# Optimization experiments

Hardware: AMD Instinct MI355X
Metric: run time of the kernel (lower is better)

The kernel has to match this reference:

```python
import math
import jax, jax.numpy as jnp
import numpy as np

DIM = 4096
N_HEADS = 32
N_KV_HEADS = 8
HEAD_DIM = DIM // N_HEADS        # 128
N_REP = N_HEADS // N_KV_HEADS    # 4
BSZ = 1
SEQ = 2048
ROPE_THETA = 500000.0


def setup_inputs() -> dict:
    key = jax.random.key(0)
    ks = jax.random.split(key, 5)
    scale = 1.0 / math.sqrt(DIM)
    x = jax.random.normal(ks[0], (BSZ, SEQ, DIM), dtype=jnp.float32)
    wq = jax.random.normal(ks[1], (N_HEADS * HEAD_DIM, DIM), dtype=jnp.float32) * scale
    wk = jax.random.normal(ks[2], (N_KV_HEADS * HEAD_DIM, DIM), dtype=jnp.float32) * scale
    wv = jax.random.normal(ks[3], (N_KV_HEADS * HEAD_DIM, DIM), dtype=jnp.float32) * scale
    wo = jax.random.normal(ks[4], (N_HEADS * HEAD_DIM, DIM), dtype=jnp.float32).T * scale
    wo = jnp.asarray(wo)  # [DIM, N_HEADS*HEAD_DIM] like nn.Linear(in=heads*hd, out=dim).weight
    # RoPE tables: freqs_cis[t, j] = exp(i * t * theta^{-2j/head_dim}), j in [0, head_dim/2)
    inv_freq = 1.0 / (ROPE_THETA ** (np.arange(0, HEAD_DIM, 2, dtype=np.float32) / HEAD_DIM))
    t = np.arange(SEQ, dtype=np.float32)
    ang = np.outer(t, inv_freq)  # [SEQ, HEAD_DIM//2]
    freqs_cos = jnp.asarray(np.cos(ang), dtype=jnp.float32)
    freqs_sin = jnp.asarray(np.sin(ang), dtype=jnp.float32)
    # additive causal mask [SEQ, SEQ]
    mask = jnp.where(jnp.tril(jnp.ones((SEQ, SEQ), dtype=bool)), 0.0, -1e9).astype(jnp.float32)
    return {"x": x, "wq": wq, "wk": wk, "wv": wv, "wo": wo,
            "freqs_cos": freqs_cos, "freqs_sin": freqs_sin, "mask": mask}


def _apply_rope(xh, cos, sin):
    # xh: [b, s, h, head_dim]; cos/sin: [s, head_dim//2]
    b, s, h, d = xh.shape
    xr = xh.reshape(b, s, h, d // 2, 2)
    x0, x1 = xr[..., 0], xr[..., 1]
    c = cos[None, :, None, :]
    sn = sin[None, :, None, :]
    o0 = x0 * c - x1 * sn
    o1 = x0 * sn + x1 * c
    return jnp.stack([o0, o1], axis=-1).reshape(b, s, h, d)


def reference(x, wq, wk, wv, wo, freqs_cos, freqs_sin, mask):
    bsz, seqlen, _ = x.shape
    xq = (x @ wq.T).reshape(bsz, seqlen, N_HEADS, HEAD_DIM)
    xk = (x @ wk.T).reshape(bsz, seqlen, N_KV_HEADS, HEAD_DIM)
    xv = (x @ wv.T).reshape(bsz, seqlen, N_KV_HEADS, HEAD_DIM)
    xq = _apply_rope(xq, freqs_cos, freqs_sin)
    xk = _apply_rope(xk, freqs_cos, freqs_sin)
    # repeat_kv (GQA expansion)
    keys = jnp.repeat(xk, N_REP, axis=2)    # [b, s, N_HEADS, hd]
    values = jnp.repeat(xv, N_REP, axis=2)
    scores = jnp.einsum('bqhd,bkhd->bhqk', xq, keys) / math.sqrt(HEAD_DIM)
    scores = scores + mask[None, None, :, :]
    scores = jax.nn.softmax(scores.astype(jnp.float32), axis=-1).astype(xq.dtype)
    out = jnp.einsum('bhqk,bkhd->bqhd', scores, values)
    out = out.reshape(bsz, seqlen, N_HEADS * HEAD_DIM)
    return out @ wo.T
```

## Files before the change

kernel.cpp:

```cpp
#include <hip/hip_runtime.h>
#include <math.h>
#include <stdint.h>
#include <stddef.h>


typedef __attribute__((ext_vector_type(8))) short bf16x8;
typedef __attribute__((ext_vector_type(4))) short bf16x4;
typedef __attribute__((ext_vector_type(4))) float f32x4;
typedef unsigned short u16;
typedef unsigned int u32;

#define NEG_BIG (-1.0e9f)
#define MFMA32(a, b, c) __builtin_amdgcn_mfma_f32_16x16x32_bf16(a, b, c, 0, 0, 0)
#define SFENCE() __builtin_amdgcn_sched_barrier(0)
#define BAR() __builtin_amdgcn_s_barrier()
#define VMW(n_) asm volatile("s_waitcnt vmcnt(" #n_ ")" ::: "memory")

__device__ __forceinline__ float bf2f(u16 b) {
    return __uint_as_float(((unsigned int)b) << 16);
}
__device__ __forceinline__ u16 f2bf(float f) {
    unsigned int u = __float_as_uint(f);
    u += 0x7fff + ((u >> 16) & 1);
    return (u16)(u >> 16);
}
__device__ __forceinline__ void gld_lds16(short* lds, const u16* g) {
    __builtin_amdgcn_global_load_lds(
        (const __attribute__((address_space(1))) void*)g,
        (__attribute__((address_space(3))) void*)lds, 16, 0, 0);
}
__device__ __forceinline__ void cvt8(const float* __restrict__ s,
                                     u16* __restrict__ d, int i) {
    float4 a, c;
    __builtin_memcpy(&a, s + i, 16);
    __builtin_memcpy(&c, s + i + 4, 16);
    bf16x8 o;
    o[0] = (short)f2bf(a.x); o[1] = (short)f2bf(a.y);
    o[2] = (short)f2bf(a.z); o[3] = (short)f2bf(a.w);
    o[4] = (short)f2bf(c.x); o[5] = (short)f2bf(c.y);
    o[6] = (short)f2bf(c.z); o[7] = (short)f2bf(c.w);
    __builtin_memcpy(d + i, &o, 16);
}

__global__ __launch_bounds__(256) void cvt_all(
    const float* __restrict__ x, const float* __restrict__ wq,
    const float* __restrict__ wk, const float* __restrict__ wv,
    u16* __restrict__ xb, u16* __restrict__ wqb, u16* __restrict__ wkb,
    u16* __restrict__ wvb) {
    const int b = blockIdx.x;
    const float* s; u16* d; int off;
    if (b < 4096)       { s = x;  d = xb;  off = b; }
    else if (b < 12288) { s = wq; d = wqb; off = b - 4096; }
    else if (b < 14336) { s = wk; d = wkb; off = b - 12288; }
    else                { s = wv; d = wvb; off = b - 14336; }
    cvt8(s, d, off * 2048 + threadIdx.x * 8);
}


#define QSTGA(bf_, ks_, kt_)                                                 \
    { _Pragma("unroll") for (int r_ = 0; r_ < 2; ++r_)                       \
        gld_lds16(Ad + (bf_) * 16384 + (ks_) * 8192 + r_ * 4096,             \
                  Ag + gK * r_ + (size_t)(kt_) * 64 + (ks_) * 32); }
#define QSTGB(bf_, ks_, kt_)                                                 \
    { _Pragma("unroll") for (int r_ = 0; r_ < 2; ++r_)                       \
        gld_lds16(Bd + (bf_) * 16384 + (ks_) * 8192 + r_ * 4096,             \
                  Bg + gK * r_ + (size_t)(kt_) * 64 + (ks_) * 32); }
#define QRDA(bank_, bf_, ks_, mh_)                                           \
    { _Pragma("unroll") for (int i_ = 0; i_ < 4; ++i_)                       \
        __builtin_memcpy(&bank_[i_], S + (bf_) * 16384 + (ks_) * 8192 +      \
                         abase + ((mh_) * 64 + i_ * 16) * 32, 16); }
#define QRDB(bank_, bf_, ks_)                                                \
    { _Pragma("unroll") for (int n_ = 0; n_ < 4; ++n_)                       \
        __builtin_memcpy(&bank_[n_], Bs + (bf_) * 16384 + (ks_) * 8192 +     \
                         bbase + n_ * 512, 16); }
#define QMM(afb_, bfb_, mh_)                                                 \
    {                                                                        \
        __builtin_amdgcn_s_setprio(1);                                       \
        _Pragma("unroll") for (int i_ = 0; i_ < 4; ++i_)                     \
            _Pragma("unroll") for (int n_ = 0; n_ < 4; ++n_)                 \
                acc[(mh_) * 4 + i_][n_] =                                    \
                    MFMA32(afb_[i_], bfb_[n_], acc[(mh_) * 4 + i_][n_]);     \
        __builtin_amdgcn_s_setprio(0);                                       \
    }

template <int OUT, int ROPE>
__device__ __forceinline__ void gemm_q(const u16* __restrict__ A,
                                       const u16* __restrict__ B,
                                       void* __restrict__ C,
                                       const float* __restrict__ fc,
                                       const float* __restrict__ fs,
                                       int mb, int nb, int N, int K,
                                       short* __restrict__ S) {
    short* const Bs = S + 32768;
    const int t = threadIdx.x;
    const int lane = t & 63, l15 = lane & 15, quad = lane >> 4;
    const int wid = t >> 6, wr = wid >> 2, wc = wid & 3;

    const int srow = t >> 2;
    const int cs = (t & 3) ^ ((t >> 3) & 3);
    const u16* const Ag = A + (size_t)(mb * 256 + srow) * K + cs * 8;
    const u16* const Bg = B + (size_t)(nb * 256 + srow) * K + cs * 8;
    short* const Ad = S + t * 8;
    short* const Bd = Bs + t * 8;
    const size_t gK = (size_t)128 * K;

    const int swz = (quad ^ ((l15 >> 1) & 3)) * 8;
    const int abase = (wr * 128 + l15) * 32 + swz;
    const int bbase = (wc * 64 + l15) * 32 + swz;

    f32x4 acc[8][4] = {};
    bf16x8 af0[4], af1[4], bf0[4], bf1[4];

    QSTGA(0, 0, 0); QSTGB(0, 0, 0);
    QSTGA(0, 1, 0); QSTGB(0, 1, 0);
    QSTGA(1, 0, 1); QSTGB(1, 0, 1);
    VMW(8);
    BAR();
    QRDA(af0, 0, 0, 0); QRDB(bf0, 0, 0);
    SFENCE();

    const int nIt = K >> 7;
    for (int it = 0; it < nIt - 1; ++it) {
        const int k1 = 2 * it + 1, kn0 = 2 * it + 2, kn1 = 2 * it + 3;
        QSTGA(1, 1, k1);  QRDA(af1, 0, 0, 1);                    QMM(af0, bf0, 0); SFENCE(); VMW(6); BAR();
        QSTGB(1, 1, k1);  QRDA(af0, 0, 1, 0); QRDB(bf1, 0, 1);   QMM(af1, bf0, 1); SFENCE();         BAR();
        QSTGA(0, 0, kn0); QRDA(af1, 0, 1, 1);                    QMM(af0, bf1, 0); SFENCE(); VMW(6); BAR();
        QSTGB(0, 0, kn0); QRDA(af0, 1, 0, 0); QRDB(bf0, 1, 0);   QMM(af1, bf1, 1); SFENCE();         BAR();
        QSTGA(0, 1, kn0); QRDA(af1, 1, 0, 1);                    QMM(af0, bf0, 0); SFENCE(); VMW(6); BAR();
        QSTGB(0, 1, kn0); QRDA(af0, 1, 1, 0); QRDB(bf1, 1, 1);   QMM(af1, bf0, 1); SFENCE();         BAR();
        QSTGA(1, 0, kn1); QRDA(af1, 1, 1, 1);                    QMM(af0, bf1, 0); SFENCE(); VMW(6); BAR();
        QSTGB(1, 0, kn1); QRDA(af0, 0, 0, 0); QRDB(bf0, 0, 0);   QMM(af1, bf1, 1); SFENCE();         BAR();
    }
    {
        const int k1 = 2 * nIt - 1;
        QSTGA(1, 1, k1);  QRDA(af1, 0, 0, 1);                    QMM(af0, bf0, 0); SFENCE(); VMW(6); BAR();
        QSTGB(1, 1, k1);  QRDA(af0, 0, 1, 0); QRDB(bf1, 0, 1);   QMM(af1, bf0, 1); SFENCE();         BAR();
        QRDA(af1, 0, 1, 1);                                      QMM(af0, bf1, 0); SFENCE(); VMW(4); BAR();
        QRDA(af0, 1, 0, 0); QRDB(bf0, 1, 0);                     QMM(af1, bf1, 1); SFENCE();         BAR();
        QRDA(af1, 1, 0, 1);                                      QMM(af0, bf0, 0); SFENCE(); VMW(0); BAR();
        QRDA(af0, 1, 1, 0); QRDB(bf1, 1, 1);                     QMM(af1, bf0, 1); SFENCE();         BAR();
        QRDA(af1, 1, 1, 1);                                      QMM(af0, bf1, 0); SFENCE();         BAR();
        QMM(af1, bf1, 1);
    }

#pragma unroll
    for (int i8 = 0; i8 < 8; ++i8) {
        const int rowb = mb * 256 + wr * 128 + (i8 >> 2) * 64 +
                         (i8 & 3) * 16 + quad * 4;
#pragma unroll
        for (int j = 0; j < 4; ++j) {
            const int col = nb * 256 + wc * 64 + j * 16 + l15;
            if (OUT == 2) {
                bf16x4 v;
#pragma unroll
                for (int r = 0; r < 4; ++r) v[r] = (short)f2bf(acc[i8][j][r]);
                __builtin_memcpy((u16*)C + (size_t)col * 2048 + rowb, &v, 8);
            } else if (ROPE) {
                const int pi = (col & 127) >> 1;
                const bool odd = (l15 & 1);
#pragma unroll
                for (int r = 0; r < 4; ++r) {
                    const int s = rowb + r;
                    const float c = fc[s * 64 + pi];
                    const float sn = fs[s * 64 + pi];
                    const float v = acc[i8][j][r];
                    const float vp = __shfl_xor(v, 1);
                    const float out = odd ? (vp * sn + v * c)
                                          : (v * c - vp * sn);
                    ((u16*)C)[(size_t)s * N + col] = f2bf(out);
                }
            } else {
#pragma unroll
                for (int r = 0; r < 4; ++r)
                    ((u16*)C)[(size_t)(rowb + r) * N + col] =
                        f2bf(acc[i8][j][r]);
            }
        }
    }
}

__global__ __launch_bounds__(512, 2) void qkv_proj8(
    const u16* __restrict__ x,
    const u16* __restrict__ wq, const u16* __restrict__ wk,
    const u16* __restrict__ wv,
    const float* __restrict__ wof, u16* __restrict__ wob,
    const float* __restrict__ fc, const float* __restrict__ fs,
    u16* __restrict__ Q, u16* __restrict__ Kc, u16* __restrict__ Vt) {
    __shared__ __align__(16) short S[65536];
    const int lid = blockIdx.x;
    if (lid >= 192) {
        const int cb = lid - 192, t = threadIdx.x;
        for (int it = 0; it < 64; ++it)
            cvt8(wof, wob, ((cb * 64 + it) * 512 + t) * 8);
        return;
    }
    const int swzb = (lid & 7) * 24 + (lid >> 3);
    const int mb = swzb & 7, y = swzb >> 3;
    if (y < 16)
        gemm_q<0, 1>(x, wq, Q, fc, fs, mb, y, 4096, 4096, S);
    else if (y < 20)
        gemm_q<0, 1>(x, wk, Kc, fc, fs, mb, y - 16, 1024, 4096, S);
    else
        gemm_q<2, 0>(x, wv, Vt, fc, fs, mb, y - 20, 1024, 4096, S);
}


#define O8_STG(bf_, ks_, kt_)                                                \
    {                                                                        \
        gld_lds16(Ad + (bf_) * 8192 + (ks_) * 4096,                          \
                  Ag + (size_t)(kt_) * 64 + (ks_) * 32);                     \
        _Pragma("unroll") for (int r_ = 0; r_ < 2; ++r_)                     \
            gld_lds16(Bd + (bf_) * 16384 + (ks_) * 8192 + r_ * 4096,         \
                      Bg + gK * r_ + (size_t)(kt_) * 64 + (ks_) * 32);       \
    }
#define O8_PHASE(bf_, ks_, STAGE_, WAIT_)                                    \
    {                                                                        \
        _Pragma("unroll") for (int n_ = 0; n_ < 4; ++n_)                     \
            __builtin_memcpy(&bfr[n_], Bs + (bf_) * 16384 + (ks_) * 8192 +   \
                                           bbase + n_ * 512, 16);            \
        _Pragma("unroll") for (int i_ = 0; i_ < 4; ++i_)                     \
            __builtin_memcpy(&af[i_], S + (bf_) * 8192 + (ks_) * 4096 +      \
                                          abase + i_ * 512, 16);             \
        STAGE_;                                                              \
        SFENCE();                                                            \
        __builtin_amdgcn_s_barrier();                                        \
        asm volatile("s_waitcnt lgkmcnt(0)" ::: "memory");                   \
        SFENCE();                                                            \
        __builtin_amdgcn_s_setprio(1);                                       \
        _Pragma("unroll") for (int i_ = 0; i_ < 4; ++i_)                     \
            _Pragma("unroll") for (int n_ = 0; n_ < 4; ++n_)                 \
                acc[i_][n_] = MFMA32(af[i_], bfr[n_], acc[i_][n_]);          \
        __builtin_amdgcn_s_setprio(0);                                       \
        SFENCE();                                                            \
        WAIT_;                                                               \
        __builtin_amdgcn_s_barrier();                                        \
    }

__global__ __launch_bounds__(512, 2) void oproj8(
    const u16* __restrict__ A, const u16* __restrict__ wo,
    float* __restrict__ out) {
    __shared__ __align__(16) short S[49152];
    short* const Bs = S + 16384;
    const int lid = blockIdx.x;
    const int logical = (lid & 7) * 32 + (lid >> 3);
    const int mb = logical & 15, nb = logical >> 4;

    const int t = threadIdx.x;
    const int lane = t & 63, l15 = lane & 15, quad = lane >> 4;
    const int wid = t >> 6, wr = wid >> 2, wc = wid & 3;

    const int srow = t >> 2;
    const int cs = (t & 3) ^ ((t >> 3) & 3);
    const u16* const Ag = A + (size_t)(mb * 128 + srow) * 4096 + cs * 8;
    const u16* const Bg = wo + (size_t)(nb * 256 + srow) * 4096 + cs * 8;
    short* const Ad = S + t * 8;
    short* const Bd = Bs + t * 8;
    const size_t gK = (size_t)128 * 4096;

    const int swz = (quad ^ ((l15 >> 1) & 3)) * 8;
    const int abase = (wr * 64 + l15) * 32 + swz;
    const int bbase = (wc * 64 + l15) * 32 + swz;

    f32x4 acc[4][4] = {};
    bf16x8 af[4], bfr[4];

    O8_STG(0, 0, 0); O8_STG(0, 1, 0); O8_STG(1, 0, 1);
    VMW(6);
    BAR();

    const int nIt = 32;
    for (int it = 0; it < nIt - 1; ++it) {
        const int k1 = 2 * it + 1, kn0 = 2 * it + 2, kn1 = 2 * it + 3;
        O8_PHASE(0, 0, O8_STG(1, 1, k1),  VMW(6));
        O8_PHASE(0, 1, O8_STG(0, 0, kn0), VMW(6));
        O8_PHASE(1, 0, O8_STG(0, 1, kn0), VMW(6));
        O8_PHASE(1, 1, O8_STG(1, 0, kn1), VMW(6));
    }
    {
        const int k1 = 2 * nIt - 1;
        O8_PHASE(0, 0, O8_STG(1, 1, k1), VMW(6));
        O8_PHASE(0, 1, ,                 VMW(3));
        O8_PHASE(1, 0, ,                 VMW(0));
        O8_PHASE(1, 1, , );
    }

#pragma unroll
    for (int i = 0; i < 4; ++i) {
        const int rowb = mb * 128 + wr * 64 + i * 16 + quad * 4;
#pragma unroll
        for (int j = 0; j < 4; ++j) {
            const int col = nb * 256 + wc * 64 + j * 16 + l15;
#pragma unroll
            for (int r = 0; r < 4; ++r)
                out[(size_t)(rowb + r) * 4096 + col] = acc[i][j][r];
        }
    }
}

__device__ __forceinline__ int kswz(int row, int cs) {
    int f = (row & 3) | ((row & 8) >> 1);
    return row * 128 + ((cs ^ f) << 3);
}

template <bool MASKED>
__device__ __forceinline__ void fa_step_lds(
    const short* __restrict__ Kl, const short* __restrict__ Vl,
    int kb, int kadd, int q0, int l15, int quad,
    const int (&koff)[8], const int (&voff)[8],
    const bf16x8 (&qf)[4], const bf16x8 vones,
    f32x4 (&o)[8], f32x4& o9, float& m) {
    const float c1 = 0.08838834764831845f * 1.4426950408889634f;

    bf16x8 kf[8];
#pragma unroll
    for (int i = 0; i < 8; ++i)
        __builtin_memcpy(&kf[i], Kl + koff[i] + kadd, 16);
    f32x4 s0 = {0, 0, 0, 0}, s1 = {0, 0, 0, 0};
#pragma unroll
    for (int c = 0; c < 4; ++c) {
        s0 = MFMA32(kf[c], qf[c], s0);
        s1 = MFMA32(kf[4 + c], qf[c], s1);
    }

    bf16x8 vf[8];
#pragma unroll
    for (int n = 0; n < 8; ++n) __builtin_memcpy(&vf[n], Vl + voff[n], 16);

    float sv0[4], sv1[4];
    const int q = q0 + l15;
#pragma unroll
    for (int r = 0; r < 4; ++r) {
        sv0[r] = s0[r];
        sv1[r] = s1[r];
        if (MASKED) {
            if (kb + 8 * quad + r > q) sv0[r] = NEG_BIG;
            if (kb + 8 * quad + 4 + r > q) sv1[r] = NEG_BIG;
        }
    }

    float mx = fmaxf(fmaxf(fmaxf(sv0[0], sv0[1]), fmaxf(sv0[2], sv0[3])),
                     fmaxf(fmaxf(sv1[0], sv1[1]), fmaxf(sv1[2], sv1[3])));
    mx = fmaxf(mx, __shfl_xor(mx, 16));
    mx = fmaxf(mx, __shfl_xor(mx, 32));

    if (!__all(mx <= m + 90.0f)) {
        float mnew = fmaxf(m, mx);
        float alpha = exp2f((m - mnew) * c1);
        float aO[4];
#pragma unroll
        for (int r = 0; r < 4; ++r) aO[r] = __shfl(alpha, quad * 20 + r);
#pragma unroll
        for (int n = 0; n < 8; ++n)
#pragma unroll
            for (int r = 0; r < 4; ++r) o[n][r] *= aO[r];
#pragma unroll
        for (int r = 0; r < 4; ++r) o9[r] *= aO[r];
        m = mnew;
    }

    const float mc = m * c1;
    float p0[4], p1[4];
#pragma unroll
    for (int r = 0; r < 4; ++r) {
        p0[r] = exp2f(__builtin_fmaf(sv0[r], c1, -mc));
        p1[r] = exp2f(__builtin_fmaf(sv1[r], c1, -mc));
    }

    u32 w0, w1, w2, w3;
    asm("v_cvt_pk_bf16_f32 %0, %1, %2" : "=v"(w0) : "v"(p0[0]), "v"(p0[1]));
    asm("v_cvt_pk_bf16_f32 %0, %1, %2" : "=v"(w1) : "v"(p0[2]), "v"(p0[3]));
    asm("v_cvt_pk_bf16_f32 %0, %1, %2" : "=v"(w2) : "v"(p1[0]), "v"(p1[1]));
    asm("v_cvt_pk_bf16_f32 %0, %1, %2" : "=v"(w3) : "v"(p1[2]), "v"(p1[3]));
    u32 wa[4] = {w0, w1, w2, w3};
    bf16x8 pa;
    __builtin_memcpy(&pa, wa, 16);

#pragma unroll
    for (int n = 0; n < 8; ++n) o[n] = MFMA32(pa, vf[n], o[n]);
    o9 = MFMA32(pa, vones, o9);
}

__device__ __forceinline__ void fa_task(
    const u16* __restrict__ Q, const u16* __restrict__ Kc,
    const u16* __restrict__ Vt, u16* __restrict__ O,
    short* __restrict__ Kl0, short* __restrict__ Vl0,
    int q0, int nbt64, int h, int kvh, int t) {
    const int lane = t & 63;
    const int l15 = lane & 15, quad = lane >> 4;

    bf16x8 qf[4];
    const u16* qp = Q + (size_t)(q0 + l15) * 4096 + h * 128 + quad * 8;
#pragma unroll
    for (int c = 0; c < 4; ++c) __builtin_memcpy(&qf[c], qp + c * 32, 16);

    bf16x8 vones;
#pragma unroll
    for (int i = 0; i < 8; ++i) vones[i] = (short)0x3F80;

    const u16* ksrc[4]; short* kdst[4];
    const u16* vsrc[4]; short* vdst[4];
#pragma unroll
    for (int r = 0; r < 4; ++r) {
        int row = (t >> 4) + 16 * r;
        int slot = t & 15;
        int f = (row & 3) | ((row & 8) >> 1);
        int cks = slot ^ f;
        ksrc[r] = Kc + (size_t)row * 1024 + kvh * 128 + cks * 8;
        kdst[r] = Kl0 + (t + 256 * r) * 8;
        int rowv = (t >> 3) + 32 * r;
        int csv = (t & 7) ^ ((t >> 3) & 7);
        vsrc[r] = Vt + (size_t)(kvh * 128 + rowv) * 2048 + csv * 8;
        vdst[r] = Vl0 + (t + 256 * r) * 8;
    }

    const int rk0 = 8 * (l15 >> 2) + (l15 & 3);
    int koff[8], voff0[8], voff1[8];
#pragma unroll
    for (int c = 0; c < 4; ++c) {
        koff[c] = kswz(rk0, quad + c * 4);
        koff[4 + c] = kswz(rk0 + 4, quad + c * 4);
    }
#pragma unroll
    for (int n = 0; n < 8; ++n) {
        const int row = n * 16 + l15;
        voff0[n] = row * 64 + ((quad ^ (l15 & 7)) << 3);
        voff1[n] = row * 64 + (((quad + 4) ^ (l15 & 7)) << 3);
    }

    f32x4 o[8] = {};
    f32x4 o9 = {0, 0, 0, 0};
    float m = NEG_BIG;
    const int my_nb32 = (q0 + 47) / 32;

#pragma unroll
    for (int r = 0; r < 4; ++r) {
        gld_lds16(kdst[r], ksrc[r]);
        gld_lds16(vdst[r], vsrc[r]);
    }
    __syncthreads();

    for (int ib = 0; ib < nbt64; ++ib) {
        if (ib + 1 < nbt64) {
            const int kb = (ib + 1) * 64;
            const int bo = ((ib + 1) & 1) * 8192;
#pragma unroll
            for (int r = 0; r < 4; ++r) {
                gld_lds16(kdst[r] + bo, ksrc[r] + (size_t)kb * 1024);
                gld_lds16(vdst[r] + bo, vsrc[r] + kb);
            }
        }
        const short* Kl = Kl0 + (ib & 1) * 8192;
        const short* Vl = Vl0 + (ib & 1) * 8192;
#pragma unroll
        for (int sub = 0; sub < 2; ++sub) {
            const int ib32 = 2 * ib + sub;
            if (ib32 < my_nb32) {
                const int kb = ib * 64 + sub * 32;
                const int kadd = sub * 4096;
                if (ib32 == my_nb32 - 1)
                    fa_step_lds<true>(Kl, Vl, kb, kadd, q0, l15, quad, koff,
                                      sub ? voff1 : voff0, qf, vones, o, o9,
                                      m);
                else
                    fa_step_lds<false>(Kl, Vl, kb, kadd, q0, l15, quad, koff,
                                       sub ? voff1 : voff0, qf, vones, o, o9,
                                       m);
            }
        }
        __syncthreads();
    }

    float inv[4];
#pragma unroll
    for (int r = 0; r < 4; ++r) inv[r] = 1.f / o9[r];
#pragma unroll
    for (int n = 0; n < 8; ++n)
#pragma unroll
        for (int r = 0; r < 4; ++r) {
            int row = q0 + quad * 4 + r;
            O[(size_t)row * 4096 + h * 128 + n * 16 + l15] =
                f2bf(o[n][r] * inv[r]);
        }
}

__global__ __launch_bounds__(256, 2) void flash_attn(
    const u16* __restrict__ Q, const u16* __restrict__ Kc,
    const u16* __restrict__ Vt, u16* __restrict__ O) {
    __shared__ __align__(16) short Kl[2 * 64 * 128];
    __shared__ __align__(16) short Vl[2 * 128 * 64];
    const int id = blockIdx.x;
    const int c = id & 7;
    const int j = id >> 3;
    const int h = 4 * c + (j & 3);
    const int pp = j >> 2;
    const int kvh = c;
    const int t = threadIdx.x, wave = t >> 6;
    fa_task(Q, Kc, Vt, O, Kl, Vl, pp * 64 + wave * 16, pp + 1, h, kvh, t);
    const int tb = 31 - pp;
    fa_task(Q, Kc, Vt, O, Kl, Vl, tb * 64 + (3 - wave) * 16, tb + 1, h,
            kvh, t);
}

extern "C" void kernel_launch(void* const* d_in, const int* in_sizes, int n_in,
                              void* d_out, int out_size, void* d_ws,
                              size_t ws_size, hipStream_t stream) {
    const float* x  = (const float*)d_in[0];
    const float* wq = (const float*)d_in[1];
    const float* wk = (const float*)d_in[2];
    const float* wv = (const float*)d_in[3];
    const float* wo = (const float*)d_in[4];
    const float* fc = (const float*)d_in[5];
    const float* fs = (const float*)d_in[6];
    float* out = (float*)d_out;

    const int NX = 2048 * 4096;
    const int NQW = 4096 * 4096;
    const int NKW = 1024 * 4096;
    const int NKV = 2048 * 1024;

    u16* Q   = (u16*)d_ws;
    u16* Kc  = Q   + NX;
    u16* Vt  = Kc  + NKV;
    u16* Ao  = Vt  + NKV;
    u16* xb  = Ao  + NX;
    u16* wqb = xb  + NX;
    u16* wkb = wqb + NQW;
    u16* wvb = wkb + NKW;
    u16* wob = wvb + NKW;

    cvt_all<<<16384, 256, 0, stream>>>(x, wq, wk, wv, xb, wqb, wkb, wvb);
    qkv_proj8<<<256, 512, 0, stream>>>(xb, wqb, wkb, wvb, wo, wob, fc, fs,
                                       Q, Kc, Vt);
    flash_attn<<<512, 256, 0, stream>>>(Q, Kc, Vt, Ao);
    oproj8<<<256, 512, 0, stream>>>(Ao, wob, out);
}
```

Baseline: 455.3 us.

## Triple-buffer output projection GEMM with register double-buffered LDS fragments

The output projection kernel moves from a two-stage to a three-stage LDS ring of k-tiles. It also double-buffers the A/B fragments in registers, so the LDS reads for the next sub-tile are issued while the current MFMAs run, with one barrier per phase instead of two. Separately, the fp32-to-bf16 conversion of wo inside the QKV kernel now uses nontemporal loads and stores. The trade-off is more LDS per block (about 144 KB) and more fragment registers, which may limit occupancy and adds a more intricate wait and barrier schedule.

```diff
diff --git a/kernel.cpp b/kernel.cpp
--- a/kernel.cpp
+++ b/kernel.cpp
@@ -40,6 +40,17 @@
     o[4] = (short)f2bf(c.x); o[5] = (short)f2bf(c.y);
     o[6] = (short)f2bf(c.z); o[7] = (short)f2bf(c.w);
     __builtin_memcpy(d + i, &o, 16);
+}
+__device__ __forceinline__ void cvt8_nt(const float* __restrict__ s,
+                                        u16* __restrict__ d, int i) {
+    f32x4 a = __builtin_nontemporal_load((const f32x4*)(s + i));
+    f32x4 c = __builtin_nontemporal_load((const f32x4*)(s + i + 4));
+    bf16x8 o;
+    o[0] = (short)f2bf(a[0]); o[1] = (short)f2bf(a[1]);
+    o[2] = (short)f2bf(a[2]); o[3] = (short)f2bf(a[3]);
+    o[4] = (short)f2bf(c[0]); o[5] = (short)f2bf(c[1]);
+    o[6] = (short)f2bf(c[2]); o[7] = (short)f2bf(c[3]);
+    __builtin_nontemporal_store(o, (bf16x8*)(d + i));
 }
 
 __global__ __launch_bounds__(256) void cvt_all(
@@ -191,7 +202,7 @@
     if (lid >= 192) {
         const int cb = lid - 192, t = threadIdx.x;
         for (int it = 0; it < 64; ++it)
-            cvt8(wof, wob, ((cb * 64 + it) * 512 + t) * 8);
+            cvt8_nt(wof, wob, ((cb * 64 + it) * 512 + t) * 8);
         return;
     }
     const int swzb = (lid & 7) * 24 + (lid >> 3);
@@ -205,7 +216,7 @@
 }
 
 
-#define O8_STG(bf_, ks_, kt_)                                                \
+#define O3_STG(bf_, ks_, kt_)                                                \
     {                                                                        \
         gld_lds16(Ad + (bf_) * 8192 + (ks_) * 4096,                          \
                   Ag + (size_t)(kt_) * 64 + (ks_) * 32);                     \
@@ -213,34 +224,29 @@
             gld_lds16(Bd + (bf_) * 16384 + (ks_) * 8192 + r_ * 4096,         \
                       Bg + gK * r_ + (size_t)(kt_) * 64 + (ks_) * 32);       \
     }
-#define O8_PHASE(bf_, ks_, STAGE_, WAIT_)                                    \
+#define O3_RD(ab_, bb_, bf_, ks_)                                            \
     {                                                                        \
+        _Pragma("unroll") for (int i_ = 0; i_ < 4; ++i_)                     \
+            __builtin_memcpy(&ab_[i_], S + (bf_) * 8192 + (ks_) * 4096 +     \
+                             abase + i_ * 512, 16);                          \
         _Pragma("unroll") for (int n_ = 0; n_ < 4; ++n_)                     \
-            __builtin_memcpy(&bfr[n_], Bs + (bf_) * 16384 + (ks_) * 8192 +   \
-                                           bbase + n_ * 512, 16);            \
-        _Pragma("unroll") for (int i_ = 0; i_ < 4; ++i_)                     \
-            __builtin_memcpy(&af[i_], S + (bf_) * 8192 + (ks_) * 4096 +      \
-                                          abase + i_ * 512, 16);             \
-        STAGE_;                                                              \
-        SFENCE();                                                            \
-        __builtin_amdgcn_s_barrier();                                        \
-        asm volatile("s_waitcnt lgkmcnt(0)" ::: "memory");                   \
-        SFENCE();                                                            \
+            __builtin_memcpy(&bb_[n_], Bs + (bf_) * 16384 + (ks_) * 8192 +   \
+                             bbase + n_ * 512, 16);                          \
+    }
+#define O3_MM(ab_, bb_)                                                      \
+    {                                                                        \
         __builtin_amdgcn_s_setprio(1);                                       \
         _Pragma("unroll") for (int i_ = 0; i_ < 4; ++i_)                     \
             _Pragma("unroll") for (int n_ = 0; n_ < 4; ++n_)                 \
-                acc[i_][n_] = MFMA32(af[i_], bfr[n_], acc[i_][n_]);          \
+                acc[i_][n_] = MFMA32(ab_[i_], bb_[n_], acc[i_][n_]);         \
         __builtin_amdgcn_s_setprio(0);                                       \
-        SFENCE();                                                            \
-        WAIT_;                                                               \
-        __builtin_amdgcn_s_barrier();                                        \
-    }
-
-__global__ __launch_bounds__(512, 2) void oproj8(
+    }
+
+__global__ __launch_bounds__(512, 2) void oproj3(
     const u16* __restrict__ A, const u16* __restrict__ wo,
     float* __restrict__ out) {
-    __shared__ __align__(16) short S[49152];
-    short* const Bs = S + 16384;
+    __shared__ __align__(16) short S[73728];
+    short* const Bs = S + 24576;
     const int lid = blockIdx.x;
     const int logical = (lid & 7) * 32 + (lid >> 3);
     const int mb = logical & 15, nb = logical >> 4;
@@ -262,27 +268,48 @@
     const int bbase = (wc * 64 + l15) * 32 + swz;
 
     f32x4 acc[4][4] = {};
-    bf16x8 af[4], bfr[4];
-
-    O8_STG(0, 0, 0); O8_STG(0, 1, 0); O8_STG(1, 0, 1);
-    VMW(6);
+    bf16x8 af0[4], af1[4], bf0[4], bf1[4];
+
+    O3_STG(0, 0, 0); O3_STG(0, 1, 0);
+    O3_STG(1, 0, 1); O3_STG(1, 1, 1);
+    O3_STG(2, 0, 2);
+    VMW(9);
     BAR();
-
-    const int nIt = 32;
-    for (int it = 0; it < nIt - 1; ++it) {
-        const int k1 = 2 * it + 1, kn0 = 2 * it + 2, kn1 = 2 * it + 3;
-        O8_PHASE(0, 0, O8_STG(1, 1, k1),  VMW(6));
-        O8_PHASE(0, 1, O8_STG(0, 0, kn0), VMW(6));
-        O8_PHASE(1, 0, O8_STG(0, 1, kn0), VMW(6));
-        O8_PHASE(1, 1, O8_STG(1, 0, kn1), VMW(6));
-    }
-    {
-        const int k1 = 2 * nIt - 1;
-        O8_PHASE(0, 0, O8_STG(1, 1, k1), VMW(6));
-        O8_PHASE(0, 1, ,                 VMW(3));
-        O8_PHASE(1, 0, ,                 VMW(0));
-        O8_PHASE(1, 1, , );
-    }
+    O3_RD(af0, bf0, 0, 0);
+    SFENCE();
+
+    for (int it = 0; it < 21; ++it) {
+        const int k0 = 3 * it, k1 = k0 + 1, k2 = k0 + 2;
+        const bool nl = (it < 20);
+        O3_STG(2, 1, k2);
+        O3_RD(af1, bf1, 0, 1); O3_MM(af0, bf0); SFENCE(); VMW(6); BAR();
+        O3_STG(0, 0, k0 + 3);
+        O3_RD(af0, bf0, 1, 0); O3_MM(af1, bf1); SFENCE(); VMW(6); BAR();
+        O3_STG(0, 1, k0 + 3);
+        O3_RD(af1, bf1, 1, 1); O3_MM(af0, bf0); SFENCE(); VMW(6); BAR();
+        if (nl) {
+            O3_STG(1, 0, k1 + 3);
+            O3_RD(af0, bf0, 2, 0); O3_MM(af1, bf1); SFENCE(); VMW(6); BAR();
+        } else {
+            O3_RD(af0, bf0, 2, 0); O3_MM(af1, bf1); SFENCE(); VMW(3); BAR();
+        }
+        if (nl) {
+            O3_STG(1, 1, k1 + 3);
+            O3_RD(af1, bf1, 2, 1); O3_MM(af0, bf0); SFENCE(); VMW(6); BAR();
+        } else {
+            O3_RD(af1, bf1, 2, 1); O3_MM(af0, bf0); SFENCE(); VMW(0); BAR();
+        }
+        if (nl) {
+            O3_STG(2, 0, k2 + 3);
+            O3_RD(af0, bf0, 0, 0); O3_MM(af1, bf1); SFENCE(); VMW(6); BAR();
+        } else {
+            O3_RD(af0, bf0, 0, 0); O3_MM(af1, bf1); SFENCE();         BAR();
+        }
+    }
+    O3_RD(af1, bf1, 0, 1);
+    O3_MM(af0, bf0);
+    SFENCE();
+    O3_MM(af1, bf1);
 
 #pragma unroll
     for (int i = 0; i < 4; ++i) {
@@ -532,5 +559,5 @@
     qkv_proj8<<<256, 512, 0, stream>>>(xb, wqb, wkb, wvb, wo, wob, fc, fs,
                                        Q, Kc, Vt);
     flash_attn<<<512, 256, 0, stream>>>(Q, Kc, Vt, Ao);
-    oproj8<<<256, 512, 0, stream>>>(Ao, wob, out);
-}
+    oproj3<<<256, 512, 0, stream>>>(Ao, wob, out);
+}
```

Measured after the change: 484.3 us. +6.4%, slower.
